# Kernel tuning notes

Measured on AMD Instinct MI355X. Metric: run time of the kernel, lower is better.

Reference implementation:

```python
import jax, jax.numpy as jnp
import numpy as np

IMAGE_SIZE = (224, 224)
SIGMA = 4.0
KS = 2 * int(4.0 * SIGMA + 0.5) + 1  # 33


def _gaussian_kernel2d(ks, sigma):
    x = jnp.arange(ks, dtype=jnp.float32) - (ks - 1) / 2.0
    g = jnp.exp(-(x ** 2) / (2.0 * sigma ** 2))
    g = g / g.sum()
    return jnp.outer(g, g)  # already sums to 1; normalize_kernel2d is a no-op


def setup_inputs() -> dict:
    key = jax.random.key(0)
    k1, k2, k3 = jax.random.split(key, 3)
    B, C, H, W = 32, 200, 56, 56
    HW = H * W
    embedding = jax.random.normal(k1, (B, C, H, W), dtype=jnp.float32)
    mean = jax.random.normal(k2, (C, HW), dtype=jnp.float32)
    A = jax.random.normal(k3, (HW, C, C), dtype=jnp.float32)
    # PSD per-pixel inverse covariance, as produced by real PaDiM statistics
    inv_covariance = jnp.einsum('nij,nkj->nik', A, A) / C + 0.1 * jnp.eye(C, dtype=jnp.float32)
    covariance = jnp.zeros((1,), dtype=jnp.float32)  # unused on mahalanobis path
    return {"embedding": embedding, "mean": mean,
            "inv_covariance": inv_covariance, "covariance": covariance}


def reference(embedding, mean, inv_covariance, covariance):
    B, C, H, W = embedding.shape
    HW = H * W
    emb = embedding.reshape(B, C, HW)
    # delta: [HW, B, C]
    delta = jnp.transpose(emb - mean[None], (2, 0, 1))
    # per-pixel mahalanobis quadratic form: diag(delta @ inv_cov @ delta^T)
    md = jnp.matmul(delta, inv_covariance)          # [HW, B, C]
    q = jnp.sum(md * delta, axis=-1)                # [HW, B]
    dist = jnp.sqrt(jnp.clip(q, 0.0, None))
    score = jnp.transpose(dist, (1, 0)).reshape(B, 1, H, W)
    # bilinear upsample (align_corners=False == half-pixel centers)
    up = jax.image.resize(score, (B, 1, IMAGE_SIZE[0], IMAGE_SIZE[1]), method='bilinear')
    # gaussian blur, reflect 'same' padding, single channel
    kernel = _gaussian_kernel2d(KS, SIGMA)[None, None]  # [1,1,KS,KS]
    pad = (KS - 1) // 2
    padded = jnp.pad(up, ((0, 0), (0, 0), (pad, pad), (pad, pad)), mode='reflect')
    out = jax.lax.conv_general_dilated(padded, kernel, window_strides=(1, 1),
                                       padding='VALID')
    return out
```

## Files before the change

kernel.cpp:

```cpp
#include <hip/hip_runtime.h>
#include <math.h>

#define HW   3136
#define NC   200
#define NB   32
#define SS   56
#define OS   224
#define KS   33
#define GPAD 16

#define KP   224
#define DP   232
#define NP   208
#define KTP  40
#define NKT  7

typedef __attribute__((ext_vector_type(8))) short   short8;
typedef __attribute__((ext_vector_type(4))) float   f32x4;

__device__ __forceinline__ unsigned short f2bf(float x) {
    unsigned int u = __builtin_bit_cast(unsigned int, x);
    u += 0x7FFFu + ((u >> 16) & 1u);
    return (unsigned short)(u >> 16);
}
__device__ __forceinline__ float bf2f(unsigned short h) {
    unsigned int u = ((unsigned int)h) << 16;
    return __builtin_bit_cast(float, u);
}

__global__ __launch_bounds__(256, 3)
void k_mahal(const float* __restrict__ emb,
             const float* __restrict__ mean,
             const float* __restrict__ icov,
             float* __restrict__ score) {
    const int bid = blockIdx.x;
    const int n = (bid & 7) * 392 + (bid >> 3);
    const int t = threadIdx.x;

    __shared__ __align__(16) unsigned short dd[NB * DP];
    __shared__ __align__(16) unsigned short bt[2][NP * KTP];
    __shared__ float qs[NB];

    const float* Mn = icov + (size_t)n * (NC * NC);

    float4 pf[7];
    {
        const float4* src = (const float4*)Mn;
#pragma unroll
        for (int i = 0; i < 7; i++) {
            int idx = t + i * 256;
            if (idx < 1600) pf[i] = src[idx];
        }
    }

    for (int idx = t; idx < NB * NC; idx += 256) {
        int b = idx / NC, c = idx - b * NC;
        float v = emb[(size_t)(b * NC + c) * HW + n] - mean[(size_t)c * HW + n];
        dd[b * DP + c] = f2bf(v);
    }
    for (int idx = t; idx < NB * 32; idx += 256) {
        int b = idx >> 5;
        dd[b * DP + NC + (idx & 31)] = 0;
    }
    for (int idx = t; idx < 2 * 8 * KTP; idx += 256) {
        int buf = idx / (8 * KTP), r = idx - buf * (8 * KTP);
        bt[buf][(NC + r / KTP) * KTP + (r % KTP)] = 0;
    }
    if (t < NB) qs[t] = 0.0f;
    __syncthreads();

    const int lane = t & 63;
    const int w    = t >> 6;
    const int col  = lane & 15;
    const int quad = lane >> 4;

    short8 aF[2][NKT];
#pragma unroll
    for (int m = 0; m < 2; m++)
#pragma unroll
        for (int kt = 0; kt < NKT; kt++)
            aF[m][kt] = *(const short8*)&dd[(m * 16 + col) * DP + kt * 32 + quad * 8];

    f32x4 acc[2][4];
#pragma unroll
    for (int m = 0; m < 2; m++)
#pragma unroll
        for (int i = 0; i < 4; i++)
            acc[m][i] = (f32x4){0.f, 0.f, 0.f, 0.f};

#pragma unroll
    for (int kt = 0; kt < NKT; kt++) {
        const int nf4 = (kt < 6) ? 1600 : 400;
        unsigned short* btc = bt[kt & 1];
#pragma unroll
        for (int i = 0; i < 7; i++) {
            int idx = t + i * 256;
            if (idx < nf4) {
                int k  = idx / 50;
                int n4 = (idx - k * 50) * 4;
                float4 f = pf[i];
                btc[(n4 + 0) * KTP + k] = f2bf(f.x);
                btc[(n4 + 1) * KTP + k] = f2bf(f.y);
                btc[(n4 + 2) * KTP + k] = f2bf(f.z);
                btc[(n4 + 3) * KTP + k] = f2bf(f.w);
            }
        }
        if (kt < NKT - 1) {
            const int nnext = (kt < 5) ? 1600 : 400;
            const float4* src = (const float4*)(Mn + (size_t)(kt + 1) * 32 * NC);
#pragma unroll
            for (int i = 0; i < 7; i++) {
                int idx = t + i * 256;
                if (idx < nnext) pf[i] = src[idx];
            }
        }
        __syncthreads();
#pragma unroll
        for (int i = 0; i < 4; i++) {
            int nt = w + 4 * i;
            if (nt < 13) {
                short8 bF = *(const short8*)&btc[(nt * 16 + col) * KTP + quad * 8];
                acc[0][i] = __builtin_amdgcn_mfma_f32_16x16x32_bf16(aF[0][kt], bF, acc[0][i], 0, 0, 0);
                acc[1][i] = __builtin_amdgcn_mfma_f32_16x16x32_bf16(aF[1][kt], bF, acc[1][i], 0, 0, 0);
            }
        }
    }

#pragma unroll
    for (int i = 0; i < 4; i++) {
        int nt = w + 4 * i;
        if (nt < 13) {
#pragma unroll
            for (int m = 0; m < 2; m++) {
                f32x4 a = acc[m][i];
#pragma unroll
                for (int r = 0; r < 4; r++) {
                    int b = m * 16 + quad * 4 + r;
                    float v = a[r] * bf2f(dd[b * DP + nt * 16 + col]);
                    v += __shfl_xor(v, 1);
                    v += __shfl_xor(v, 2);
                    v += __shfl_xor(v, 4);
                    v += __shfl_xor(v, 8);
                    if (col == 0) atomicAdd(&qs[b], v);
                }
            }
        }
    }
    __syncthreads();
    if (t < NB) {
        float q = qs[t];
        score[(size_t)t * HW + n] = sqrtf(q > 0.f ? q : 0.f);
    }
}

__global__ void k_upsample(const float* __restrict__ score,
                           float* __restrict__ up) {
    int idx = blockIdx.x * 256 + threadIdx.x;
    if (idx >= NB * OS * OS) return;
    int x = idx % OS;
    int y = (idx / OS) % OS;
    int b = idx / (OS * OS);

    float sy = 0.25f * y - 0.375f;
    float sx = 0.25f * x - 0.375f;
    int y0 = (int)floorf(sy); float fy = sy - (float)y0;
    int x0 = (int)floorf(sx); float fx = sx - (float)x0;
    int y0c = min(max(y0, 0), SS - 1), y1c = min(max(y0 + 1, 0), SS - 1);
    int x0c = min(max(x0, 0), SS - 1), x1c = min(max(x0 + 1, 0), SS - 1);

    const float* sb = score + (size_t)b * HW;
    float v00 = sb[y0c * SS + x0c];
    float v01 = sb[y0c * SS + x1c];
    float v10 = sb[y1c * SS + x0c];
    float v11 = sb[y1c * SS + x1c];
    up[idx] = (1.f - fy) * ((1.f - fx) * v00 + fx * v01) +
              fy * ((1.f - fx) * v10 + fx * v11);
}

__global__ void k_gauss_init(float* __restrict__ g) {
    if (threadIdx.x == 0) {
        float e[KS];
        float sum = 0.f;
        for (int i = 0; i < KS; i++) {
            float x = (float)i - 16.0f;
            e[i] = expf(-(x * x) / 32.0f);
            sum += e[i];
        }
        for (int i = 0; i < KS; i++) g[i] = e[i] / sum;
    }
}

__device__ __forceinline__ int reflect224(int i) {
    if (i < 0) return -i;
    if (i > OS - 1) return 2 * (OS - 1) - i;
    return i;
}

__global__ void k_hblur(const float* __restrict__ up,
                        const float* __restrict__ g,
                        float* __restrict__ tmp) {
    int idx = blockIdx.x * 256 + threadIdx.x;
    if (idx >= NB * OS * OS) return;
    int x = idx % OS;
    int row = idx / OS;
    const float* src = up + (size_t)row * OS;
    float acc = 0.f;
#pragma unroll
    for (int t = -GPAD; t <= GPAD; t++) {
        acc += g[t + GPAD] * src[reflect224(x + t)];
    }
    tmp[idx] = acc;
}

__global__ void k_vblur(const float* __restrict__ tmp,
                        const float* __restrict__ g,
                        float* __restrict__ out) {
    int idx = blockIdx.x * 256 + threadIdx.x;
    if (idx >= NB * OS * OS) return;
    int x = idx % OS;
    int y = (idx / OS) % OS;
    int b = idx / (OS * OS);
    const float* src = tmp + (size_t)b * OS * OS;
    float acc = 0.f;
#pragma unroll
    for (int t = -GPAD; t <= GPAD; t++) {
        acc += g[t + GPAD] * src[(size_t)reflect224(y + t) * OS + x];
    }
    out[idx] = acc;
}

extern "C" void kernel_launch(void* const* d_in, const int* in_sizes, int n_in,
                              void* d_out, int out_size, void* d_ws, size_t ws_size,
                              hipStream_t stream) {
    const float* emb  = (const float*)d_in[0];
    const float* mean = (const float*)d_in[1];
    const float* icov = (const float*)d_in[2];
    float* out = (float*)d_out;

    char* ws = (char*)d_ws;
    float* g     = (float*)ws;
    float* score = (float*)(ws + 256);
    float* tmp   = (float*)(ws + 256 + 401408);

    const int up_blocks = (NB * OS * OS) / 256;

    k_gauss_init<<<1, 64, 0, stream>>>(g);
    k_mahal<<<HW, 256, 0, stream>>>(emb, mean, icov, score);
    k_upsample<<<up_blocks, 256, 0, stream>>>(score, out);
    k_hblur<<<up_blocks, 256, 0, stream>>>(out, g, tmp);
    k_vblur<<<up_blocks, 256, 0, stream>>>(tmp, g, out);
}
```

Measured before the change: 850.7 us.

## Split delta into coalesced pre-pass and stream icov via async LDS loads

Adds a k_delta kernel that computes emb-mean with coalesced tile loads and writes bf16 deltas in an MFMA-ready per-pixel layout, replacing the strided per-pixel gather inside the Mahalanobis kernel. The main kernel now streams icov rows with global_load_lds into a double-buffered fp32 slab, converts to bf16 on the fly, and swaps MFMA operand roles so icov rows form the A operand. The quadratic form is reduced per 16-row chunk rather than in a final epilogue. This adds an extra kernel launch and a workspace round trip for the deltas, plus per-iteration barriers.

```diff
diff --git a/kernel.cpp b/kernel.cpp
--- a/kernel.cpp
+++ b/kernel.cpp
@@ -9,14 +9,9 @@
 #define KS   33
 #define GPAD 16
 
-#define KP   224
-#define DP   232
-#define NP   208
-#define KTP  40
-#define NKT  7
-
-typedef __attribute__((ext_vector_type(8))) short   short8;
-typedef __attribute__((ext_vector_type(4))) float   f32x4;
+typedef __attribute__((ext_vector_type(8))) short          short8;
+typedef __attribute__((ext_vector_type(4))) float          f32x4;
+typedef __attribute__((ext_vector_type(4))) unsigned short ush4;
 
 __device__ __forceinline__ unsigned short f2bf(float x) {
     unsigned int u = __builtin_bit_cast(unsigned int, x);
@@ -28,124 +23,165 @@
     return __builtin_bit_cast(float, u);
 }
 
-__global__ __launch_bounds__(256, 3)
-void k_mahal(const float* __restrict__ emb,
+__device__ __forceinline__ void gload16(const void* g, void* l) {
+    __builtin_amdgcn_global_load_lds(
+        (const __attribute__((address_space(1))) void*)g,
+        (__attribute__((address_space(3))) void*)l, 16, 0, 0);
+}
+
+__global__ __launch_bounds__(256)
+void k_delta(const float* __restrict__ emb,
              const float* __restrict__ mean,
-             const float* __restrict__ icov,
-             float* __restrict__ score) {
+             unsigned short* __restrict__ dg) {
+    const int tile = blockIdx.x >> 2;
+    const int bq   = blockIdx.x & 3;
+    const int n0   = tile * 16;
+    const int t    = threadIdx.x;
+
+    __shared__ float          mm[32 * 20];
+    __shared__ unsigned short tr[256 * 20];
+
+    unsigned int* dgU = (unsigned int*)dg;
+
+    for (int kt = 0; kt < 7; kt++) {
+        const int c0 = kt * 32;
+        if (t < 128) {
+            int cl = t >> 2, nl4 = (t & 3) * 4;
+            int c = c0 + cl;
+            float4 v = {0.f, 0.f, 0.f, 0.f};
+            if (c < NC) v = *(const float4*)&mean[(size_t)c * HW + n0 + nl4];
+            *(float4*)&mm[cl * 20 + nl4] = v;
+        }
+        __syncthreads();
+#pragma unroll
+        for (int j = 0; j < 4; j++) {
+            int row = (t >> 2) + 64 * j;
+            int nl4 = (t & 3) * 4;
+            int b   = bq * 8 + (row >> 5);
+            int cl  = row & 31;
+            int c   = c0 + cl;
+            ush4 wv = {0, 0, 0, 0};
+            if (c < NC) {
+                float4 e = *(const float4*)&emb[((size_t)(b * NC + c)) * HW + n0 + nl4];
+                float4 m = *(const float4*)&mm[cl * 20 + nl4];
+                wv[0] = f2bf(e.x - m.x); wv[1] = f2bf(e.y - m.y);
+                wv[2] = f2bf(e.z - m.z); wv[3] = f2bf(e.w - m.w);
+            }
+            *(ush4*)&tr[row * 20 + nl4] = wv;
+        }
+        __syncthreads();
+#pragma unroll
+        for (int j = 0; j < 8; j++) {
+            int idx = t + 256 * j;
+            int nl  = idx >> 7, rem = idx & 127;
+            int bl  = rem >> 4, cu = rem & 15;
+            int cb  = bl * 32 + 2 * cu;
+            unsigned int lo = tr[cb * 20 + nl];
+            unsigned int hi = tr[(cb + 1) * 20 + nl];
+            dgU[((size_t)(n0 + nl) * 7 + kt) * 512 +
+                (size_t)(bq * 8 + bl) * 16 + cu] = lo | (hi << 16);
+        }
+        __syncthreads();
+    }
+}
+
+__global__ __launch_bounds__(256, 4)
+void k_mahal2(const unsigned short* __restrict__ dg,
+              const float* __restrict__ icov,
+              float* __restrict__ score) {
     const int bid = blockIdx.x;
     const int n = (bid & 7) * 392 + (bid >> 3);
     const int t = threadIdx.x;
 
-    __shared__ __align__(16) unsigned short dd[NB * DP];
-    __shared__ __align__(16) unsigned short bt[2][NP * KTP];
+    __shared__ unsigned short dd[7 * 1024];
+    __shared__ float slab[2][16 * NC];
     __shared__ float qs[NB];
 
-    const float* Mn = icov + (size_t)n * (NC * NC);
-
-    float4 pf[7];
+    const float* Mn   = icov + (size_t)n * (NC * NC);
+    const char*  dsrc = (const char*)(dg + (size_t)n * 7168);
+
     {
-        const float4* src = (const float4*)Mn;
-#pragma unroll
-        for (int i = 0; i < 7; i++) {
-            int idx = t + i * 256;
-            if (idx < 1600) pf[i] = src[idx];
-        }
-    }
-
-    for (int idx = t; idx < NB * NC; idx += 256) {
-        int b = idx / NC, c = idx - b * NC;
-        float v = emb[(size_t)(b * NC + c) * HW + n] - mean[(size_t)c * HW + n];
-        dd[b * DP + c] = f2bf(v);
-    }
-    for (int idx = t; idx < NB * 32; idx += 256) {
-        int b = idx >> 5;
-        dd[b * DP + NC + (idx & 31)] = 0;
-    }
-    for (int idx = t; idx < 2 * 8 * KTP; idx += 256) {
-        int buf = idx / (8 * KTP), r = idx - buf * (8 * KTP);
-        bt[buf][(NC + r / KTP) * KTP + (r % KTP)] = 0;
-    }
-    if (t < NB) qs[t] = 0.0f;
+        char* lb = (char*)dd;
+#pragma unroll
+        for (int i = 0; i < 4; i++) {
+            int idx = i * 256 + t;
+            if (idx < 896)
+                gload16(dsrc + (size_t)idx * 16, lb + (i * 256 + (t & 192)) * 16);
+        }
+        const char* ms = (const char*)Mn;
+        char* sb = (char*)&slab[0][0];
+#pragma unroll
+        for (int i = 0; i < 4; i++) {
+            int idx = i * 256 + t;
+            if (idx < 800)
+                gload16(ms + (size_t)idx * 16, sb + (i * 256 + (t & 192)) * 16);
+        }
+    }
+    if (t < NB) qs[t] = 0.f;
     __syncthreads();
 
     const int lane = t & 63;
     const int w    = t >> 6;
     const int col  = lane & 15;
     const int quad = lane >> 4;
-
-    short8 aF[2][NKT];
-#pragma unroll
-    for (int m = 0; m < 2; m++)
-#pragma unroll
-        for (int kt = 0; kt < NKT; kt++)
-            aF[m][kt] = *(const short8*)&dd[(m * 16 + col) * DP + kt * 32 + quad * 8];
-
-    f32x4 acc[2][4];
-#pragma unroll
-    for (int m = 0; m < 2; m++)
-#pragma unroll
-        for (int i = 0; i < 4; i++)
-            acc[m][i] = (f32x4){0.f, 0.f, 0.f, 0.f};
-
-#pragma unroll
-    for (int kt = 0; kt < NKT; kt++) {
-        const int nf4 = (kt < 6) ? 1600 : 400;
-        unsigned short* btc = bt[kt & 1];
-#pragma unroll
-        for (int i = 0; i < 7; i++) {
-            int idx = t + i * 256;
-            if (idx < nf4) {
-                int k  = idx / 50;
-                int n4 = (idx - k * 50) * 4;
-                float4 f = pf[i];
-                btc[(n4 + 0) * KTP + k] = f2bf(f.x);
-                btc[(n4 + 1) * KTP + k] = f2bf(f.y);
-                btc[(n4 + 2) * KTP + k] = f2bf(f.z);
-                btc[(n4 + 3) * KTP + k] = f2bf(f.w);
+    const int bt   = w & 1;
+    const int kg   = w >> 1;
+    const int nk   = kg ? 3 : 4;
+    const int ddb  = (bt * 16 + col) * 32;
+
+    short8 bF[4];
+#pragma unroll
+    for (int q = 0; q < 4; q++) {
+        if (q < nk) {
+            int kt = kg + 2 * q;
+            bF[q] = *(const short8*)&dd[kt * 1024 + ddb + quad * 8];
+        }
+    }
+
+    const int abase = col * NC + quad * 8;
+    float qacc = 0.f;
+
+    for (int it = 0; it < 13; it++) {
+        if (it < 12) {
+            const int nf4 = (it == 11) ? 400 : 800;
+            const char* ms = (const char*)(Mn + (size_t)(it + 1) * 16 * NC);
+            char* sb = (char*)&slab[(it + 1) & 1][0];
+#pragma unroll
+            for (int i = 0; i < 4; i++) {
+                int idx = i * 256 + t;
+                if (idx < nf4)
+                    gload16(ms + (size_t)idx * 16, sb + (i * 256 + (t & 192)) * 16);
             }
         }
-        if (kt < NKT - 1) {
-            const int nnext = (kt < 5) ? 1600 : 400;
-            const float4* src = (const float4*)(Mn + (size_t)(kt + 1) * 32 * NC);
-#pragma unroll
-            for (int i = 0; i < 7; i++) {
-                int idx = t + i * 256;
-                if (idx < nnext) pf[i] = src[idx];
+        const float* sl = &slab[it & 1][0];
+        f32x4 acc = {0.f, 0.f, 0.f, 0.f};
+#pragma unroll
+        for (int q = 0; q < 4; q++) {
+            if (q < nk) {
+                int kt = kg + 2 * q;
+                const f32x4* ap = (const f32x4*)&sl[abase + kt * 32];
+                f32x4 lo = ap[0], hi = ap[1];
+                short8 aF;
+                aF[0] = f2bf(lo[0]); aF[1] = f2bf(lo[1]);
+                aF[2] = f2bf(lo[2]); aF[3] = f2bf(lo[3]);
+                aF[4] = f2bf(hi[0]); aF[5] = f2bf(hi[1]);
+                aF[6] = f2bf(hi[2]); aF[7] = f2bf(hi[3]);
+                acc = __builtin_amdgcn_mfma_f32_16x16x32_bf16(aF, bF[q], acc, 0, 0, 0);
             }
         }
-        __syncthreads();
-#pragma unroll
-        for (int i = 0; i < 4; i++) {
-            int nt = w + 4 * i;
-            if (nt < 13) {
-                short8 bF = *(const short8*)&btc[(nt * 16 + col) * KTP + quad * 8];
-                acc[0][i] = __builtin_amdgcn_mfma_f32_16x16x32_bf16(aF[0][kt], bF, acc[0][i], 0, 0, 0);
-                acc[1][i] = __builtin_amdgcn_mfma_f32_16x16x32_bf16(aF[1][kt], bF, acc[1][i], 0, 0, 0);
-            }
-        }
-    }
-
-#pragma unroll
-    for (int i = 0; i < 4; i++) {
-        int nt = w + 4 * i;
-        if (nt < 13) {
-#pragma unroll
-            for (int m = 0; m < 2; m++) {
-                f32x4 a = acc[m][i];
-#pragma unroll
-                for (int r = 0; r < 4; r++) {
-                    int b = m * 16 + quad * 4 + r;
-                    float v = a[r] * bf2f(dd[b * DP + nt * 16 + col]);
-                    v += __shfl_xor(v, 1);
-                    v += __shfl_xor(v, 2);
-                    v += __shfl_xor(v, 4);
-                    v += __shfl_xor(v, 8);
-                    if (col == 0) atomicAdd(&qs[b], v);
-                }
-            }
-        }
-    }
+        {
+            int off = (it >> 1) * 1024 + ddb + (it & 1) * 16 + quad * 4;
+            ush4 dv = *(const ush4*)&dd[off];
+            float v = acc[0] * bf2f(dv[0]) + acc[1] * bf2f(dv[1]) +
+                      acc[2] * bf2f(dv[2]) + acc[3] * bf2f(dv[3]);
+            v += __shfl_xor(v, 16);
+            v += __shfl_xor(v, 32);
+            qacc += v;
+        }
+        __syncthreads();
+    }
+
+    if (quad == 0) atomicAdd(&qs[bt * 16 + col], qacc);
     __syncthreads();
     if (t < NB) {
         float q = qs[t];
@@ -241,11 +277,13 @@
     float* g     = (float*)ws;
     float* score = (float*)(ws + 256);
     float* tmp   = (float*)(ws + 256 + 401408);
+    unsigned short* dg = (unsigned short*)(ws + 6824192);
 
     const int up_blocks = (NB * OS * OS) / 256;
 
     k_gauss_init<<<1, 64, 0, stream>>>(g);
-    k_mahal<<<HW, 256, 0, stream>>>(emb, mean, icov, score);
+    k_delta<<<784, 256, 0, stream>>>(emb, mean, dg);
+    k_mahal2<<<HW, 256, 0, stream>>>(dg, icov, score);
     k_upsample<<<up_blocks, 256, 0, stream>>>(score, out);
     k_hblur<<<up_blocks, 256, 0, stream>>>(out, g, tmp);
     k_vblur<<<up_blocks, 256, 0, stream>>>(tmp, g, out);
```

Measured after the change: 752.4 us. -11.6%, faster.
